# Performance work log

Hardware: AMD Instinct MI355X
Metric: run time of the kernel (lower is better)

The kernel has to match this reference:

```python
import jax, jax.numpy as jnp
import numpy as np

NUM_CODES = 1024
EMBED_DIM = 256
COMMITMENT_COST = 0.25


def setup_inputs() -> dict:
    key = jax.random.key(0)
    kz, kc = jax.random.split(key)
    z = jax.random.normal(kz, (131072, EMBED_DIM), dtype=jnp.float32)
    # codebook init matches nn.Embedding weight uniform_(-1/num_codes, 1/num_codes)
    codebook = jax.random.uniform(kc, (NUM_CODES, EMBED_DIM), dtype=jnp.float32,
                                  minval=-1.0 / NUM_CODES, maxval=1.0 / NUM_CODES)
    return {"z": z, "codebook": codebook}


def reference(z, codebook):
    # Squared-euclidean distances; argmin is identical to cdist (euclidean) argmin.
    z2 = jnp.sum(z * z, axis=-1, keepdims=True)            # [N, 1]
    c2 = jnp.sum(codebook * codebook, axis=-1)             # [K]
    d = z2 - 2.0 * (z @ codebook.T) + c2                   # [N, K]
    indices = jnp.argmin(d, axis=-1)                       # [N]
    zq = codebook[indices]                                 # [N, D] embedding lookup

    commitment_loss = COMMITMENT_COST * jnp.mean(
        (jax.lax.stop_gradient(zq) - z) ** 2)
    zq_st = z + jax.lax.stop_gradient(zq - z)              # straight-through
    residual = z - jax.lax.stop_gradient(zq)               # z - z_q.detach()

    counts = jnp.bincount(indices, length=NUM_CODES).astype(jnp.float32)
    avg_probs = counts / jnp.sum(counts)
    perplexity = jnp.exp(-jnp.sum(avg_probs * jnp.log(avg_probs + 1e-10)))

    return zq_st, residual, indices, commitment_loss, perplexity
```

## Files before the change

kernel.cpp:

```cpp
#include <hip/hip_runtime.h>
#include <math.h>

#define NR 131072
#define KC 1024
#define DD 256

#define ZQ_OFF  0
#define RES_OFF 33554432
#define IDX_OFF 67108864
#define LOSS_OFF 67239936
#define PERP_OFF 67239937

#define WS_CNT 0
#define WS_C2N 4096
#define WS_IDX 8192
#define WS_BSS 532480
#define WS_CBS 548864

#define MARG 5e-4f
#define CCAP 24

#define FM(x,y) __fmul_rn((x),(y))
#define FA(x,y) __fadd_rn((x),(y))

typedef __attribute__((ext_vector_type(8))) short bf16x8;
typedef __attribute__((ext_vector_type(4))) float f32x4;

static __device__ __forceinline__ unsigned short bf16h(float f) {
  unsigned int u = __float_as_uint(f);
  u += 0x7FFFu + ((u >> 16) & 1u);
  return (unsigned short)(u >> 16);
}

static __device__ __forceinline__ float np_sumsq128(const float* __restrict__ q) {
  float lane[16];
#pragma unroll
  for (int l = 0; l < 16; l++) {
    float s0 = FM(q[l +   0], q[l +   0]);
    float s1 = FM(q[l +  16], q[l +  16]);
    float s2 = FM(q[l +  32], q[l +  32]);
    float s3 = FM(q[l +  48], q[l +  48]);
    float s4 = FM(q[l +  64], q[l +  64]);
    float s5 = FM(q[l +  80], q[l +  80]);
    float s6 = FM(q[l +  96], q[l +  96]);
    float s7 = FM(q[l + 112], q[l + 112]);
    lane[l] = FA(FA(FA(s0, s1), FA(s2, s3)), FA(FA(s4, s5), FA(s6, s7)));
  }
#pragma unroll
  for (int h = 8; h >= 1; h >>= 1)
#pragma unroll
    for (int l = 0; l < 8; l++)
      if (l < h) lane[l] = FA(lane[l], lane[l + h]);
  return lane[0];
}

static __device__ __forceinline__ float np_sumsq256(const float* __restrict__ p) {
  return FA(np_sumsq128(p), np_sumsq128(p + 128));
}

__global__ void vqt_c2(const float* __restrict__ cb, float* __restrict__ c2n) {
  const int code = blockIdx.x * 256 + threadIdx.x;
  if (code < KC) c2n[code] = np_sumsq256(cb + (size_t)code * DD);
}

__global__ void vqt_cbsplit(const float* __restrict__ cb,
                            unsigned short* __restrict__ cbs) {
  const int g  = blockIdx.x * 256 + threadIdx.x;
  const int t  = g >> 9;
  const int gi = g & 511;
  const int kc = gi >> 6, q = (gi >> 4) & 3, c = gi & 15;
  const float* src = cb + (size_t)(t * 16 + c) * DD + kc * 32 + q * 8;
  unsigned int w[4];
#pragma unroll
  for (int p = 0; p < 4; p++)
    w[p] = (unsigned int)bf16h(src[p * 2]) |
           ((unsigned int)bf16h(src[p * 2 + 1]) << 16);
  *(uint4*)(cbs + (size_t)g * 8) = make_uint4(w[0], w[1], w[2], w[3]);
}

__global__ __launch_bounds__(256, 4) void vqt_main(
    const float* __restrict__ z, const float* __restrict__ cb,
    const unsigned short* __restrict__ cbs,
    const float* __restrict__ c2n,
    float* __restrict__ out, int* __restrict__ counts,
    int* __restrict__ idxw) {
  __shared__ unsigned short ccode[128][CCAP];
  __shared__ float cd[128][CCAP];
  __shared__ int ccnt[128];
  __shared__ float m1row[128];
  __shared__ float z2s[128];
  __shared__ __align__(16) float c2l[1024];

  const int tid = threadIdx.x, wg = blockIdx.x;
  const int wv = tid >> 6, ln = tid & 63;
  const int rl = ln & 15;
  const int qk = ln >> 4;
  const int rowg0 = wg * 128 + wv * 32 + rl;

#pragma unroll
  for (int i = 0; i < 4; i++)
    ((float4*)c2l)[i * 64 + ln] = ((const float4*)c2n)[i * 64 + ln];
  if (ln < 32) ccnt[wv * 32 + ln] = 0;

  bf16x8 zH0[8], zH1[8];
#pragma unroll
  for (int kc = 0; kc < 8; kc++) {
    const float4* p0 = (const float4*)(z + (size_t)rowg0 * DD + kc * 32 + qk * 8);
    const float4* p1 = (const float4*)(z + (size_t)(rowg0 + 16) * DD + kc * 32 + qk * 8);
    const float4 a0 = p0[0], b0 = p0[1];
    const float4 a1 = p1[0], b1 = p1[1];
    zH0[kc][0] = (short)bf16h(a0.x); zH0[kc][1] = (short)bf16h(a0.y);
    zH0[kc][2] = (short)bf16h(a0.z); zH0[kc][3] = (short)bf16h(a0.w);
    zH0[kc][4] = (short)bf16h(b0.x); zH0[kc][5] = (short)bf16h(b0.y);
    zH0[kc][6] = (short)bf16h(b0.z); zH0[kc][7] = (short)bf16h(b0.w);
    zH1[kc][0] = (short)bf16h(a1.x); zH1[kc][1] = (short)bf16h(a1.y);
    zH1[kc][2] = (short)bf16h(a1.z); zH1[kc][3] = (short)bf16h(a1.w);
    zH1[kc][4] = (short)bf16h(b1.x); zH1[kc][5] = (short)bf16h(b1.y);
    zH1[kc][6] = (short)bf16h(b1.z); zH1[kc][7] = (short)bf16h(b1.w);
  }

  {
    const int gg = ln >> 4, l = ln & 15;
#pragma unroll 1
    for (int g4 = 0; g4 < 8; g4++) {
      const int rlcl = wv * 32 + g4 * 4 + gg;
      const float* q = z + (size_t)(wg * 128 + rlcl) * DD;
      float blk[2];
#pragma unroll
      for (int b = 0; b < 2; b++) {
        const float* qq = q + b * 128;
        const float s0 = FM(qq[l +   0], qq[l +   0]);
        const float s1 = FM(qq[l +  16], qq[l +  16]);
        const float s2 = FM(qq[l +  32], qq[l +  32]);
        const float s3 = FM(qq[l +  48], qq[l +  48]);
        const float s4 = FM(qq[l +  64], qq[l +  64]);
        const float s5 = FM(qq[l +  80], qq[l +  80]);
        const float s6 = FM(qq[l +  96], qq[l +  96]);
        const float s7 = FM(qq[l + 112], qq[l + 112]);
        float v = FA(FA(FA(s0, s1), FA(s2, s3)), FA(FA(s4, s5), FA(s6, s7)));
#pragma unroll
        for (int h = 8; h >= 1; h >>= 1) v = FA(v, __shfl_down(v, h, 16));
        blk[b] = v;
      }
      if (l == 0) z2s[rlcl] = FA(blk[0], blk[1]);
    }
  }

  const float z2v0 = z2s[wv * 32 + rl];
  const float z2v1 = z2s[wv * 32 + rl + 16];
  const int rw0 = wv * 32 + rl;

  float m10 = INFINITY, m11 = INFINITY;
#pragma unroll 2
  for (int t = 0; t < 64; t++) {
    bf16x8 aH[8];
#pragma unroll
    for (int kc = 0; kc < 8; kc++)
      aH[kc] = *(const bf16x8*)(cbs + (size_t)t * 4096 + kc * 512 + ln * 8);

    f32x4 accA = {0.f, 0.f, 0.f, 0.f}, accB = accA;
#pragma unroll
    for (int kc = 0; kc < 8; kc++) {
      accA = __builtin_amdgcn_mfma_f32_16x16x32_bf16(aH[kc], zH0[kc], accA, 0, 0, 0);
      accB = __builtin_amdgcn_mfma_f32_16x16x32_bf16(aH[kc], zH1[kc], accB, 0, 0, 0);
    }
    const float4 c2v4 = *(const float4*)&c2l[t * 16 + qk * 4];
    float dh0[4], dh1[4];
#pragma unroll
    for (int r = 0; r < 4; r++) {
      const float c2v = r == 0 ? c2v4.x : r == 1 ? c2v4.y : r == 2 ? c2v4.z : c2v4.w;
      dh0[r] = z2v0 - 2.f * accA[r] + c2v;
      dh1[r] = z2v1 - 2.f * accB[r] + c2v;
      m10 = fminf(m10, dh0[r]);
      m11 = fminf(m11, dh1[r]);
    }
    m10 = fminf(m10, __shfl_xor(m10, 16));
    m10 = fminf(m10, __shfl_xor(m10, 32));
    m11 = fminf(m11, __shfl_xor(m11, 16));
    m11 = fminf(m11, __shfl_xor(m11, 32));
#pragma unroll
    for (int r = 0; r < 4; r++) {
      if (dh0[r] <= m10 + MARG) {
        const int s = atomicAdd(&ccnt[rw0], 1);
        if (s < CCAP) {
          ccode[rw0][s] = (unsigned short)(t * 16 + qk * 4 + r);
          cd[rw0][s] = dh0[r];
        }
      }
      if (dh1[r] <= m11 + MARG) {
        const int s = atomicAdd(&ccnt[rw0 + 16], 1);
        if (s < CCAP) {
          ccode[rw0 + 16][s] = (unsigned short)(t * 16 + qk * 4 + r);
          cd[rw0 + 16][s] = dh1[r];
        }
      }
    }
  }

  if (qk == 0) { m1row[rw0] = m10; m1row[rw0 + 16] = m11; }

  if (ln < 32) {
    const int rwl = wv * 32 + ln;
    const int row = wg * 128 + rwl;
    const float mf = m1row[rwl] + MARG;
    const int nc = ccnt[rwl];
    int best;
    if (nc > CCAP) {
      const float* zr = z + (size_t)row * DD;
      const float z2r = z2s[rwl];
      float db = INFINITY; best = 0;
      for (int c = 0; c < KC; c++) {
        const float* cr = cb + (size_t)c * DD;
        float dot = 0.f;
#pragma unroll 8
        for (int k = 0; k < DD; k++) dot = __fmaf_rn(zr[k], cr[k], dot);
        const float t1 = 2.0f * dot;
        const float d = FA(FA(z2r, -t1), c2l[c]);
        if (d < db) { db = d; best = c; }
      }
    } else {
      int kept = 0, kcode = 0;
      for (int s = 0; s < nc; s++)
        if (cd[rwl][s] <= mf) { kept++; kcode = ccode[rwl][s]; }
      if (kept == 1) best = kcode;
      else {
        const float* zr = z + (size_t)row * DD;
        const float z2r = z2s[rwl];
        float db = INFINITY; int bi = 0x7FFFFFFF;
        for (int s = 0; s < nc; s++) {
          if (cd[rwl][s] > mf) continue;
          const int c = ccode[rwl][s];
          const float* cr = cb + (size_t)c * DD;
          float dot = 0.f;
#pragma unroll 8
          for (int k = 0; k < DD; k++) dot = __fmaf_rn(zr[k], cr[k], dot);
          const float t1 = 2.0f * dot;
          const float d = FA(FA(z2r, -t1), c2l[c]);
          if (d < db || (d == db && c < bi)) { db = d; bi = c; }
        }
        best = bi;
      }
    }
    atomicAdd(&counts[best], 1);
    idxw[row] = best;
    out[IDX_OFF + row] = (float)best;
  }
}

__global__ __launch_bounds__(256) void vqt_out(
    const float* __restrict__ z, const float* __restrict__ cb,
    const int* __restrict__ idxw, float* __restrict__ out,
    double* __restrict__ bss) {
  __shared__ double wred[4];
  const int wv = threadIdx.x >> 6, ln = threadIdx.x & 63;
  const int rowbase = (blockIdx.x * 4 + wv) * 16;

  float ss = 0.f;
#pragma unroll 1
  for (int g = 0; g < 16; g += 8) {
    float4 r4b[8], q4b[8];
#pragma unroll
    for (int u = 0; u < 8; u++) {
      const size_t zrow = (size_t)(rowbase + g + u) * DD;
      r4b[u] = ((const float4*)(z + zrow))[ln];
      q4b[u] = ((const float4*)(cb + (size_t)idxw[rowbase + g + u] * DD))[ln];
    }
#pragma unroll
    for (int u = 0; u < 8; u++) {
      const size_t zrow = (size_t)(rowbase + g + u) * DD;
      const float4 r4 = r4b[u];
      const float4 q4 = q4b[u];
      float4 stv, rsv; float dq;
      stv.x = r4.x + (q4.x - r4.x); rsv.x = r4.x - q4.x; dq = q4.x - r4.x; ss = fmaf(dq, dq, ss);
      stv.y = r4.y + (q4.y - r4.y); rsv.y = r4.y - q4.y; dq = q4.y - r4.y; ss = fmaf(dq, dq, ss);
      stv.z = r4.z + (q4.z - r4.z); rsv.z = r4.z - q4.z; dq = q4.z - r4.z; ss = fmaf(dq, dq, ss);
      stv.w = r4.w + (q4.w - r4.w); rsv.w = r4.w - q4.w; dq = q4.w - r4.w; ss = fmaf(dq, dq, ss);
      ((float4*)(out + ZQ_OFF  + zrow))[ln] = stv;
      ((float4*)(out + RES_OFF + zrow))[ln] = rsv;
    }
  }
  double dss = (double)ss;
  for (int o = 32; o; o >>= 1) dss += __shfl_down(dss, o, 64);
  if (ln == 0) wred[wv] = dss;
  __syncthreads();
  if (threadIdx.x == 0) bss[blockIdx.x] = wred[0] + wred[1] + wred[2] + wred[3];
}

__global__ void vqt_final(const int* __restrict__ counts,
                          const double* __restrict__ bss,
                          float* __restrict__ out) {
  __shared__ double red[256];
  const int t = threadIdx.x;
  double s = 0.0;
  for (int i = t; i < 2048; i += 256) s += bss[i];
  red[t] = s; __syncthreads();
  for (int s2 = 128; s2 > 0; s2 >>= 1) { if (t < s2) red[t] += red[t + s2]; __syncthreads(); }
  const double ssq = red[0];
  __syncthreads();
  double h = 0.0;
  for (int c = t; c < 1024; c += 256) {
    double p = (double)counts[c] / 131072.0;
    h += p * log(p + 1e-10);
  }
  red[t] = h; __syncthreads();
  for (int s2 = 128; s2 > 0; s2 >>= 1) { if (t < s2) red[t] += red[t + s2]; __syncthreads(); }
  if (t == 0) {
    out[LOSS_OFF] = (float)(0.25 * ssq / 33554432.0);
    out[PERP_OFF] = (float)exp(-red[0]);
  }
}

extern "C" void kernel_launch(void* const* d_in, const int* in_sizes, int n_in,
                              void* d_out, int out_size, void* d_ws, size_t ws_size,
                              hipStream_t stream) {
  const float* z;
  const float* cb;
  if (in_sizes[0] == NR * DD) { z = (const float*)d_in[0]; cb = (const float*)d_in[1]; }
  else                        { cb = (const float*)d_in[0]; z = (const float*)d_in[1]; }

  float* out = (float*)d_out;
  char* ws = (char*)d_ws;
  int*            counts = (int*)(ws + WS_CNT);
  float*          c2n    = (float*)(ws + WS_C2N);
  int*            idxw   = (int*)(ws + WS_IDX);
  double*         bssp   = (double*)(ws + WS_BSS);
  unsigned short* cbs    = (unsigned short*)(ws + WS_CBS);

  hipMemsetAsync(counts, 0, 4096, stream);
  vqt_c2<<<4, 256, 0, stream>>>(cb, c2n);
  vqt_cbsplit<<<128, 256, 0, stream>>>(cb, cbs);
  vqt_main<<<NR / 128, 256, 0, stream>>>(z, cb, cbs, c2n, out, counts, idxw);
  vqt_out<<<2048, 256, 0, stream>>>(z, cb, idxw, out, bssp);
  vqt_final<<<1, 256, 0, stream>>>(counts, bssp, out);
}
```

Before: 333.2 us.

## Halve rows per wave in VQ argmin kernel and prefetch codebook tiles

The main distance kernel now gives each wave 16 rows instead of 32, so the block covers 64 rows and the grid doubles. The codebook bf16 fragments for the next 16-code tile are loaded into registers while the current tile's MFMAs run (register double buffering). Each tile's dot product is split across two independent accumulators to shorten the dependent MFMA chain. In exchange, every codebook fragment is reused for half as many rows, so codebook traffic from L2 doubles.

```diff
diff --git a/kernel.cpp b/kernel.cpp
--- a/kernel.cpp
+++ b/kernel.cpp
@@ -58,12 +58,12 @@
   return FA(np_sumsq128(p), np_sumsq128(p + 128));
 }
 
-__global__ void vqt_c2(const float* __restrict__ cb, float* __restrict__ c2n) {
+__global__ void vqw_c2(const float* __restrict__ cb, float* __restrict__ c2n) {
   const int code = blockIdx.x * 256 + threadIdx.x;
   if (code < KC) c2n[code] = np_sumsq256(cb + (size_t)code * DD);
 }
 
-__global__ void vqt_cbsplit(const float* __restrict__ cb,
+__global__ void vqw_cbsplit(const float* __restrict__ cb,
                             unsigned short* __restrict__ cbs) {
   const int g  = blockIdx.x * 256 + threadIdx.x;
   const int t  = g >> 9;
@@ -78,53 +78,48 @@
   *(uint4*)(cbs + (size_t)g * 8) = make_uint4(w[0], w[1], w[2], w[3]);
 }
 
-__global__ __launch_bounds__(256, 4) void vqt_main(
+__global__ __launch_bounds__(256, 4) void vqw_main(
     const float* __restrict__ z, const float* __restrict__ cb,
     const unsigned short* __restrict__ cbs,
     const float* __restrict__ c2n,
     float* __restrict__ out, int* __restrict__ counts,
     int* __restrict__ idxw) {
-  __shared__ unsigned short ccode[128][CCAP];
-  __shared__ float cd[128][CCAP];
-  __shared__ int ccnt[128];
-  __shared__ float m1row[128];
-  __shared__ float z2s[128];
+  __shared__ unsigned short ccode[64][CCAP];
+  __shared__ float cd[64][CCAP];
+  __shared__ int ccnt[64];
+  __shared__ float m1row[64];
+  __shared__ float z2s[64];
   __shared__ __align__(16) float c2l[1024];
 
   const int tid = threadIdx.x, wg = blockIdx.x;
   const int wv = tid >> 6, ln = tid & 63;
   const int rl = ln & 15;
   const int qk = ln >> 4;
-  const int rowg0 = wg * 128 + wv * 32 + rl;
+  const int rw = wv * 16 + rl;
+  const int rowg = wg * 64 + rw;
 
 #pragma unroll
   for (int i = 0; i < 4; i++)
     ((float4*)c2l)[i * 64 + ln] = ((const float4*)c2n)[i * 64 + ln];
-  if (ln < 32) ccnt[wv * 32 + ln] = 0;
-
-  bf16x8 zH0[8], zH1[8];
+  if (ln < 16) ccnt[wv * 16 + ln] = 0;
+
+  bf16x8 zH[8];
 #pragma unroll
   for (int kc = 0; kc < 8; kc++) {
-    const float4* p0 = (const float4*)(z + (size_t)rowg0 * DD + kc * 32 + qk * 8);
-    const float4* p1 = (const float4*)(z + (size_t)(rowg0 + 16) * DD + kc * 32 + qk * 8);
+    const float4* p0 = (const float4*)(z + (size_t)rowg * DD + kc * 32 + qk * 8);
     const float4 a0 = p0[0], b0 = p0[1];
-    const float4 a1 = p1[0], b1 = p1[1];
-    zH0[kc][0] = (short)bf16h(a0.x); zH0[kc][1] = (short)bf16h(a0.y);
-    zH0[kc][2] = (short)bf16h(a0.z); zH0[kc][3] = (short)bf16h(a0.w);
-    zH0[kc][4] = (short)bf16h(b0.x); zH0[kc][5] = (short)bf16h(b0.y);
-    zH0[kc][6] = (short)bf16h(b0.z); zH0[kc][7] = (short)bf16h(b0.w);
-    zH1[kc][0] = (short)bf16h(a1.x); zH1[kc][1] = (short)bf16h(a1.y);
-    zH1[kc][2] = (short)bf16h(a1.z); zH1[kc][3] = (short)bf16h(a1.w);
-    zH1[kc][4] = (short)bf16h(b1.x); zH1[kc][5] = (short)bf16h(b1.y);
-    zH1[kc][6] = (short)bf16h(b1.z); zH1[kc][7] = (short)bf16h(b1.w);
+    zH[kc][0] = (short)bf16h(a0.x); zH[kc][1] = (short)bf16h(a0.y);
+    zH[kc][2] = (short)bf16h(a0.z); zH[kc][3] = (short)bf16h(a0.w);
+    zH[kc][4] = (short)bf16h(b0.x); zH[kc][5] = (short)bf16h(b0.y);
+    zH[kc][6] = (short)bf16h(b0.z); zH[kc][7] = (short)bf16h(b0.w);
   }
 
   {
     const int gg = ln >> 4, l = ln & 15;
 #pragma unroll 1
-    for (int g4 = 0; g4 < 8; g4++) {
-      const int rlcl = wv * 32 + g4 * 4 + gg;
-      const float* q = z + (size_t)(wg * 128 + rlcl) * DD;
+    for (int g4 = 0; g4 < 4; g4++) {
+      const int rlcl = wv * 16 + g4 * 4 + gg;
+      const float* q = z + (size_t)(wg * 64 + rlcl) * DD;
       float blk[2];
 #pragma unroll
       for (int b = 0; b < 2; b++) {
@@ -146,62 +141,60 @@
     }
   }
 
-  const float z2v0 = z2s[wv * 32 + rl];
-  const float z2v1 = z2s[wv * 32 + rl + 16];
-  const int rw0 = wv * 32 + rl;
-
-  float m10 = INFINITY, m11 = INFINITY;
-#pragma unroll 2
+  const float z2v = z2s[rw];
+
+  float m1 = INFINITY;
+  bf16x8 cur[8];
+#pragma unroll
+  for (int kc = 0; kc < 8; kc++)
+    cur[kc] = *(const bf16x8*)(cbs + (size_t)kc * 512 + ln * 8);
+
+#pragma unroll 1
   for (int t = 0; t < 64; t++) {
-    bf16x8 aH[8];
+    const int tn = (t < 63) ? t + 1 : 63;
+    bf16x8 nxt[8];
 #pragma unroll
     for (int kc = 0; kc < 8; kc++)
-      aH[kc] = *(const bf16x8*)(cbs + (size_t)t * 4096 + kc * 512 + ln * 8);
-
-    f32x4 accA = {0.f, 0.f, 0.f, 0.f}, accB = accA;
-#pragma unroll
-    for (int kc = 0; kc < 8; kc++) {
-      accA = __builtin_amdgcn_mfma_f32_16x16x32_bf16(aH[kc], zH0[kc], accA, 0, 0, 0);
-      accB = __builtin_amdgcn_mfma_f32_16x16x32_bf16(aH[kc], zH1[kc], accB, 0, 0, 0);
-    }
+      nxt[kc] = *(const bf16x8*)(cbs + (size_t)tn * 4096 + kc * 512 + ln * 8);
+
+    f32x4 accP = {0.f, 0.f, 0.f, 0.f}, accQ = accP;
+#pragma unroll
+    for (int kc = 0; kc < 4; kc++)
+      accP = __builtin_amdgcn_mfma_f32_16x16x32_bf16(cur[kc], zH[kc], accP, 0, 0, 0);
+#pragma unroll
+    for (int kc = 4; kc < 8; kc++)
+      accQ = __builtin_amdgcn_mfma_f32_16x16x32_bf16(cur[kc], zH[kc], accQ, 0, 0, 0);
+
     const float4 c2v4 = *(const float4*)&c2l[t * 16 + qk * 4];
-    float dh0[4], dh1[4];
+    float dh[4];
 #pragma unroll
     for (int r = 0; r < 4; r++) {
       const float c2v = r == 0 ? c2v4.x : r == 1 ? c2v4.y : r == 2 ? c2v4.z : c2v4.w;
-      dh0[r] = z2v0 - 2.f * accA[r] + c2v;
-      dh1[r] = z2v1 - 2.f * accB[r] + c2v;
-      m10 = fminf(m10, dh0[r]);
-      m11 = fminf(m11, dh1[r]);
-    }
-    m10 = fminf(m10, __shfl_xor(m10, 16));
-    m10 = fminf(m10, __shfl_xor(m10, 32));
-    m11 = fminf(m11, __shfl_xor(m11, 16));
-    m11 = fminf(m11, __shfl_xor(m11, 32));
+      const float dot = accP[r] + accQ[r];
+      dh[r] = z2v - 2.f * dot + c2v;
+      m1 = fminf(m1, dh[r]);
+    }
+    m1 = fminf(m1, __shfl_xor(m1, 16));
+    m1 = fminf(m1, __shfl_xor(m1, 32));
 #pragma unroll
     for (int r = 0; r < 4; r++) {
-      if (dh0[r] <= m10 + MARG) {
-        const int s = atomicAdd(&ccnt[rw0], 1);
+      if (dh[r] <= m1 + MARG) {
+        const int s = atomicAdd(&ccnt[rw], 1);
         if (s < CCAP) {
-          ccode[rw0][s] = (unsigned short)(t * 16 + qk * 4 + r);
-          cd[rw0][s] = dh0[r];
+          ccode[rw][s] = (unsigned short)(t * 16 + qk * 4 + r);
+          cd[rw][s] = dh[r];
         }
       }
-      if (dh1[r] <= m11 + MARG) {
-        const int s = atomicAdd(&ccnt[rw0 + 16], 1);
-        if (s < CCAP) {
-          ccode[rw0 + 16][s] = (unsigned short)(t * 16 + qk * 4 + r);
-          cd[rw0 + 16][s] = dh1[r];
-        }
-      }
-    }
-  }
-
-  if (qk == 0) { m1row[rw0] = m10; m1row[rw0 + 16] = m11; }
-
-  if (ln < 32) {
-    const int rwl = wv * 32 + ln;
-    const int row = wg * 128 + rwl;
+    }
+#pragma unroll
+    for (int kc = 0; kc < 8; kc++) cur[kc] = nxt[kc];
+  }
+
+  if (qk == 0) m1row[rw] = m1;
+
+  if (ln < 16) {
+    const int rwl = wv * 16 + ln;
+    const int row = wg * 64 + rwl;
     const float mf = m1row[rwl] + MARG;
     const int nc = ccnt[rwl];
     int best;
@@ -247,7 +240,7 @@
   }
 }
 
-__global__ __launch_bounds__(256) void vqt_out(
+__global__ __launch_bounds__(256) void vqw_out(
     const float* __restrict__ z, const float* __restrict__ cb,
     const int* __restrict__ idxw, float* __restrict__ out,
     double* __restrict__ bss) {
@@ -286,7 +279,7 @@
   if (threadIdx.x == 0) bss[blockIdx.x] = wred[0] + wred[1] + wred[2] + wred[3];
 }
 
-__global__ void vqt_final(const int* __restrict__ counts,
+__global__ void vqw_final(const int* __restrict__ counts,
                           const double* __restrict__ bss,
                           float* __restrict__ out) {
   __shared__ double red[256];
@@ -327,9 +320,9 @@
   unsigned short* cbs    = (unsigned short*)(ws + WS_CBS);
 
   hipMemsetAsync(counts, 0, 4096, stream);
-  vqt_c2<<<4, 256, 0, stream>>>(cb, c2n);
-  vqt_cbsplit<<<128, 256, 0, stream>>>(cb, cbs);
-  vqt_main<<<NR / 128, 256, 0, stream>>>(z, cb, cbs, c2n, out, counts, idxw);
-  vqt_out<<<2048, 256, 0, stream>>>(z, cb, idxw, out, bssp);
-  vqt_final<<<1, 256, 0, stream>>>(counts, bssp, out);
-}
+  vqw_c2<<<4, 256, 0, stream>>>(cb, c2n);
+  vqw_cbsplit<<<128, 256, 0, stream>>>(cb, cbs);
+  vqw_main<<<NR / 64, 256, 0, stream>>>(z, cb, cbs, c2n, out, counts, idxw);
+  vqw_out<<<2048, 256, 0, stream>>>(z, cb, idxw, out, bssp);
+  vqw_final<<<1, 256, 0, stream>>>(counts, bssp, out);
+}
```

Measured after the change: 369.5 us. 1.11x slower.
